# Kernel tuning notes

Hardware: AMD Instinct MI355X
Metric: run time of the kernel (lower is better)

## Reference

```python
import jax, jax.numpy as jnp
import numpy as np

N = 3072
F_IN = 512
H1 = 256
HFC = 64
OUT_DIM = 16
NUM_POOL = 3
P_CUT = 30.0  # ps[0]: percentile threshold on positive attention entries
CC_ITERS = 16  # min-label propagation w/ pointer jumping; reach >= 2^16 hops


def l2norm(x):
    # torch F.normalize(p=2, dim=1)
    return x / jnp.clip(jnp.linalg.norm(x, axis=1, keepdims=True), 1e-12, None)


def gcn(x, adj, W, b):
    # standard Kipf GraphConvolution: adj @ (x @ W) + b
    return adj @ (x @ W) + b


def normalize_adj(adj, k):
    n = adj.shape[0]
    A = adj + k * jnp.eye(n, dtype=adj.dtype)
    D = jnp.sqrt(A.sum(0))
    return A / (D[:, None] * D[None, :])


def edge_score(x, adj, a, W, b):
    h = x @ W + b                               # (n, HFC)
    s1 = h @ a[:HFC]                            # (n,)
    s2 = h @ a[HFC:]
    e = jax.nn.sigmoid(s1[:, None] + s2[None, :])
    att = jnp.where(adj > 0, e, jnp.zeros((), e.dtype))
    att = 0.5 * (att + att.T)
    i = jnp.arange(att.shape[0])
    return att.at[i, i].set(1.0)


def percentile_pos(att, p):
    # np.percentile(att[att>0], p) with linear interpolation, jit-safe
    pos = att > 0
    n_pos = pos.sum()
    s = jnp.sort(jnp.where(pos, att, jnp.inf).ravel())
    idx = (n_pos - 1).astype(att.dtype) * (p / 100.0)
    lo = jnp.floor(idx).astype(jnp.int32)
    hi = jnp.ceil(idx).astype(jnp.int32)
    frac = idx - lo.astype(att.dtype)
    return s[lo] * (1.0 - frac) + s[hi] * frac


def cc_labels(mask):
    # connected components via min-label propagation + pointer jumping.
    # diag of mask is always True (att diag = 1), so every node has a neighbor.
    n = mask.shape[0]
    def step(labels, _):
        neigh = jnp.min(jnp.where(mask, labels[None, :], n), axis=1)
        new = jnp.minimum(labels, neigh)
        new = new[new]  # pointer jumping doubles reach each iter
        return new, None
    labels, _ = jax.lax.scan(step, jnp.arange(n, dtype=jnp.int32), None, length=CC_ITERS)
    return labels


def pool(x, adj, att, p):
    cut = percentile_pos(att, p)
    att = att * (att >= cut).astype(att.dtype)
    labels = jax.lax.stop_gradient(cc_labels(att > 0))
    # fixed-shape membership: cluster id = representative (min) node index, padded to N
    C = jax.nn.one_hot(labels, att.shape[0], dtype=x.dtype).T  # (n_clusters=n, n)
    a2 = C @ adj @ C.T
    a2 = 0.5 * (a2 + a2.T)
    cnt = (att > 0).sum(1).astype(x.dtype)  # >=1 since diag survives the cut
    x2 = C @ ((att / cnt[:, None]) @ x)
    return x2, a2, C


def forward(x, adjC, adj, encW0, encb0, encW, encb, fcW, fcb, aW, decW, decb, decW_out, decb_out):
    adjs = [adj]
    adjCs = [adjC]
    xs, Cs, atts = [], [], []
    # ----- encode -----
    for k in range(NUM_POOL):
        x1 = x
        W, b = (encW0, encb0) if k == 0 else (encW[k - 1], encb[k - 1])
        h = jax.nn.relu(gcn(x, adjCs[-1], W, b))
        x = l2norm(h) if k == 0 else l2norm(h + x1)  # residual added for layer idx > 0
        xs.append(x)
        att = edge_score(x, adjs[-1], aW[k], fcW[k], fcb[k])
        x, adjk, C = pool(x, adjs[-1], att, P_CUT)
        adjCk = normalize_adj(adjk, 1.0)  # pool's adjC output is discarded in the original
        x = l2norm(x)
        adjs.append(adjk)
        adjCs.append(adjCk)
        atts.append(att)
        Cs.append(C)
    x = l2norm(jax.nn.elu(gcn(x, adjCs[-1], encW[NUM_POOL - 1], encb[NUM_POOL - 1])))
    xs.append(x)
    # ----- decode -----
    for k in range(NUM_POOL):
        lev = NUM_POOL - k - 1
        x = Cs[lev].T @ x                       # unpool; C is already binary
        x = jnp.concatenate([x, xs[lev]], axis=1)
        x = l2norm(jax.nn.elu(gcn(x, adjCs[lev], decW[k], decb[k])))
    x = gcn(x, adjCs[0], decW_out, decb_out)
    logp = jax.nn.log_softmax(x, axis=1)
    return logp, jnp.stack(Cs), jnp.stack(atts)


def setup_inputs() -> dict:
    key = jax.random.key(0)
    ks = jax.random.split(key, 12)
    x = jax.random.normal(ks[0], (N, F_IN), jnp.float32)
    u = jax.random.uniform(ks[1], (N, N))
    m = (u < 16.0 / N).astype(jnp.float32)  # avg degree ~16
    adj = jnp.maximum(m, m.T)
    i = jnp.arange(N)
    adj = adj.at[i, i].set(1.0)
    adjC = normalize_adj(adj, 1.0)

    def xav(k, shape):
        fan_in = shape[-2] if len(shape) > 1 else shape[-1]
        return jax.random.normal(k, shape, jnp.float32) * (1.0 / np.sqrt(fan_in))

    return {
        "x": x, "adjC": adjC, "adj": adj,
        "encW0": xav(ks[2], (F_IN, H1)), "encb0": jnp.zeros((H1,), jnp.float32),
        "encW": xav(ks[3], (NUM_POOL, H1, H1)), "encb": jnp.zeros((NUM_POOL, H1), jnp.float32),
        "fcW": xav(ks[4], (NUM_POOL, H1, HFC)), "fcb": jnp.zeros((NUM_POOL, HFC), jnp.float32),
        "aW": xav(ks[5], (NUM_POOL, 2 * HFC)),
        "decW": xav(ks[6], (NUM_POOL, 2 * H1, H1)), "decb": jnp.zeros((NUM_POOL, H1), jnp.float32),
        "decW_out": xav(ks[7], (H1, OUT_DIM)), "decb_out": jnp.zeros((OUT_DIM,), jnp.float32),
    }


def reference(x, adjC, adj, encW0, encb0, encW, encb, fcW, fcb, aW, decW, decb, decW_out, decb_out):
    return forward(x, adjC, adj, encW0, encb0, encW, encb, fcW, fcb, aW, decW, decb, decW_out, decb_out)
```

## Files before the change

kernel.cpp:

```cpp
#include <hip/hip_runtime.h>
#include <math.h>

#define NN 3072
#define FF 256
#define CAPE (1<<18)
#define MAXCH 3200

struct Scal {
  int nnzS, nnz2, nzero, mtot, ncht;
  int lo, hi, rank_rem, below_acc, c_le;
  unsigned prefix, vlo, minabove;
  float frac, cut;
};

__device__ __forceinline__ float sigm(float x){ return 1.0f/(1.0f+expf(-x)); }

__global__ __launch_bounds__(256) void k_count_dense(const float* __restrict__ A, int* __restrict__ rowcnt, float* __restrict__ Drow){
  int i=blockIdx.x, t=threadIdx.x;
  int c=0; float sm=0.f;
  for(int j=t;j<NN;j+=256){ float a=A[(size_t)i*NN+j]; if(a!=0.0f||j==i) c++; sm+=a; }
  __shared__ int s[256]; __shared__ float fs[256];
  s[t]=c; fs[t]=sm; __syncthreads();
  for(int o=128;o;o>>=1){ if(t<o){ s[t]+=s[t+o]; fs[t]+=fs[t+o]; } __syncthreads(); }
  if(t==0){ rowcnt[i]=s[0]; if(Drow) Drow[i]=sqrtf(fs[0]+1.0f); }
}

__global__ __launch_bounds__(1024) void k_scan(const int* __restrict__ cnt, int* __restrict__ rp, int* __restrict__ total){
  int t=threadIdx.x;
  int a0=cnt[t*3+0], a1=cnt[t*3+1], a2=cnt[t*3+2];
  int loc=a0+a1+a2;
  __shared__ int s[1024];
  s[t]=loc; __syncthreads();
  for(int o=1;o<1024;o<<=1){ int v=(t>=o)?s[t-o]:0; __syncthreads(); s[t]+=v; __syncthreads(); }
  int excl=s[t]-loc;
  rp[t*3+0]=excl; rp[t*3+1]=excl+a0; rp[t*3+2]=excl+a0+a1;
  if(t==1023){ rp[NN]=s[t]; *total=s[t]; }
}

__global__ __launch_bounds__(256) void k_fill_dense(const float* __restrict__ A, const float* __restrict__ ACd, const float* __restrict__ D,
    const int* __restrict__ rp, int* __restrict__ rows, int* __restrict__ cols, float* __restrict__ aval, float* __restrict__ acval){
  int i=blockIdx.x, t=threadIdx.x;
  const int CH=NN/256;
  int j0=t*CH; int c=0;
  for(int u=0;u<CH;u++){ int j=j0+u; float a=A[(size_t)i*NN+j]; if(a!=0.0f||j==i) c++; }
  __shared__ int s[256]; s[t]=c; __syncthreads();
  for(int o=1;o<256;o<<=1){ int v=(t>=o)?s[t-o]:0; __syncthreads(); s[t]+=v; __syncthreads(); }
  int pos=rp[i]+s[t]-c;
  float Di = D?D[i]:0.0f;
  for(int u=0;u<CH;u++){ int j=j0+u; float a=A[(size_t)i*NN+j];
    if(a!=0.0f||j==i){
      if(pos<CAPE){
        rows[pos]=i; cols[pos]=j; aval[pos]=a;
        acval[pos]= ACd? ACd[(size_t)i*NN+j] : (a+(j==i?1.0f:0.0f))/(Di*D[j]);
      }
      pos++;
    }
  }
}

__global__ __launch_bounds__(256) void k_gemm(const float* __restrict__ A, const float* __restrict__ B, float* __restrict__ C,
                                              int M, int K, int Nc){
  __shared__ float As[16][68];
  __shared__ float Bs[16][68];
  int tid=threadIdx.x;
  int tx=tid&15, ty=tid>>4;
  int bm=blockIdx.y*64, bn=blockIdx.x*64;
  int lm=tid>>2, lk=(tid&3)*4;
  int kr=tid>>4, nf=(tid&15)*4;
  float acc[4][4]={};
  for(int k0=0;k0<K;k0+=16){
    float4 a4=*(const float4*)(A+(size_t)(bm+lm)*K+k0+lk);
    As[lk+0][lm]=a4.x; As[lk+1][lm]=a4.y; As[lk+2][lm]=a4.z; As[lk+3][lm]=a4.w;
    float4 b4=*(const float4*)(B+(size_t)(k0+kr)*Nc+bn+nf);
    *(float4*)&Bs[kr][nf]=b4;
    __syncthreads();
#pragma unroll
    for(int kk=0;kk<16;kk++){
      float4 av=*(const float4*)&As[kk][ty*4];
      float4 bv=*(const float4*)&Bs[kk][tx*4];
      float am[4]={av.x,av.y,av.z,av.w};
      float bb[4]={bv.x,bv.y,bv.z,bv.w};
#pragma unroll
      for(int i2=0;i2<4;i2++)
#pragma unroll
        for(int j2=0;j2<4;j2++) acc[i2][j2]+=am[i2]*bb[j2];
    }
    __syncthreads();
  }
  for(int i2=0;i2<4;i2++){
    float4 o=make_float4(acc[i2][0],acc[i2][1],acc[i2][2],acc[i2][3]);
    *(float4*)(C+(size_t)(bm+ty*4+i2)*Nc+bn+tx*4)=o;
  }
}

__global__ __launch_bounds__(256) void k_gemm16(const float* __restrict__ X, const float* __restrict__ W, float* __restrict__ T){
  int idx=blockIdx.x*256+threadIdx.x;
  if(idx>=NN*16) return;
  int i=idx>>4, o=idx&15;
  float s=0.f;
  for(int kk=0;kk<FF;kk++) s+=X[(size_t)i*FF+kk]*W[kk*16+o];
  T[idx]=s;
}

__global__ __launch_bounds__(256) void k_spmm_gcn(const int* __restrict__ rp, const int* __restrict__ cols, const float* __restrict__ vals,
    const float* __restrict__ X, const float* __restrict__ bias, const float* __restrict__ resid, float* __restrict__ out, int act){
  int wid=blockIdx.x*4+(threadIdx.x>>6);
  int lane=threadIdx.x&63;
  if(wid>=NN) return;
  int e0=rp[wid], e1=rp[wid+1];
  float4 acc=make_float4(0,0,0,0);
  for(int e=e0;e<e1;e++){
    float v=vals[e]; int c=cols[e];
    float4 xv=*(const float4*)(X+(size_t)c*FF+lane*4);
    acc.x+=v*xv.x; acc.y+=v*xv.y; acc.z+=v*xv.z; acc.w+=v*xv.w;
  }
  float4 bv=*(const float4*)(bias+lane*4);
  acc.x+=bv.x; acc.y+=bv.y; acc.z+=bv.z; acc.w+=bv.w;
  if(act==0){
    acc.x=fmaxf(acc.x,0.f); acc.y=fmaxf(acc.y,0.f); acc.z=fmaxf(acc.z,0.f); acc.w=fmaxf(acc.w,0.f);
  } else {
    acc.x=acc.x>0.f?acc.x:expm1f(acc.x); acc.y=acc.y>0.f?acc.y:expm1f(acc.y);
    acc.z=acc.z>0.f?acc.z:expm1f(acc.z); acc.w=acc.w>0.f?acc.w:expm1f(acc.w);
  }
  if(resid){
    float4 r=*(const float4*)(resid+(size_t)wid*FF+lane*4);
    acc.x+=r.x; acc.y+=r.y; acc.z+=r.z; acc.w+=r.w;
  }
  float ss=acc.x*acc.x+acc.y*acc.y+acc.z*acc.z+acc.w*acc.w;
  for(int o=32;o;o>>=1) ss+=__shfl_xor(ss,o);
  float nrm=fmaxf(sqrtf(ss),1e-12f);
  float4 o4=make_float4(acc.x/nrm,acc.y/nrm,acc.z/nrm,acc.w/nrm);
  *(float4*)(out+(size_t)wid*FF+lane*4)=o4;
}

__global__ __launch_bounds__(256) void k_spmm_plain(const int* __restrict__ rp, const int* __restrict__ cols, const float* __restrict__ vals,
    const float* __restrict__ X, float* __restrict__ out){
  int wid=blockIdx.x*4+(threadIdx.x>>6);
  int lane=threadIdx.x&63;
  if(wid>=NN) return;
  int e0=rp[wid], e1=rp[wid+1];
  float4 acc=make_float4(0,0,0,0);
  for(int e=e0;e<e1;e++){
    if(e>=CAPE) break;
    float v=vals[e]; int c=cols[e];
    float4 xv=*(const float4*)(X+(size_t)c*FF+lane*4);
    acc.x+=v*xv.x; acc.y+=v*xv.y; acc.z+=v*xv.z; acc.w+=v*xv.w;
  }
  *(float4*)(out+(size_t)wid*FF+lane*4)=acc;
}

__global__ __launch_bounds__(64) void k_edge(const float* __restrict__ X, const float* __restrict__ fw, const float* __restrict__ fb,
    const float* __restrict__ av, float* __restrict__ s1, float* __restrict__ s2, Scal* sc){
  int i=blockIdx.x, l=threadIdx.x;
  if(i==0&&l==0) sc->nzero=0;
  __shared__ float xr[FF];
  *(float4*)&xr[l*4]=*(const float4*)(X+(size_t)i*FF+l*4);
  __syncthreads();
  float h=fb[l];
  for(int kk=0;kk<FF;kk++) h+=xr[kk]*fw[kk*64+l];
  float p1=h*av[l], p2=h*av[64+l];
  for(int o=32;o;o>>=1){ p1+=__shfl_xor(p1,o); p2+=__shfl_xor(p2,o); }
  if(l==0){ s1[i]=p1; s2[i]=p2; }
}

__global__ __launch_bounds__(256) void k_att_row(const int* __restrict__ rp, const int* __restrict__ cols,
    const float* __restrict__ s1, const float* __restrict__ s2, float* __restrict__ attD, float* __restrict__ cand, Scal* sc){
  __shared__ float row[NN];
  __shared__ int wred[4];
  int i=blockIdx.x, t=threadIdx.x;
  for(int j=t;j<NN;j+=256) row[j]=0.f;
  __syncthreads();
  int e0=rp[i], e1=rp[i+1];
  float s1i=s1[i], s2i=s2[i];
  int nz=0;
  for(int e=e0+t;e<e1;e+=256){
    int j=cols[e];
    float v=(j==i)?1.0f:0.5f*(sigm(s1i+s2[j])+sigm(s1[j]+s2i));
    row[j]=v;
    if(e<CAPE) cand[e]=v;
    if(!(v>0.f)) nz++;
  }
  for(int o=32;o;o>>=1) nz+=__shfl_xor(nz,o);
  if((t&63)==0) wred[t>>6]=nz;
  __syncthreads();
  if(t==0){ int s=wred[0]+wred[1]+wred[2]+wred[3]; if(s) atomicAdd(&sc->nzero,s); }
  float* orow=attD+(size_t)i*NN;
  for(int j=t*4;j<NN;j+=1024) *(float4*)(orow+j)=*(const float4*)&row[j];
}

__global__ void k_prep(Scal* sc){
  int np=sc->nnzS - sc->nzero;
  float idx=(float)(np-1)*(30.0f/100.0f);
  float fl=floorf(idx), ce=ceilf(idx);
  sc->lo=(int)fl; sc->hi=(int)ce; sc->frac=idx-fl;
  sc->rank_rem=sc->lo;
  sc->below_acc=0;
  sc->minabove=0xFFFFFFFFu;
}

template<int PHASE>
__global__ __launch_bounds__(256) void k_hist(const float* __restrict__ cand, const Scal* __restrict__ sc, unsigned* __restrict__ bins){
  const int NB = (PHASE==0)?16384:256;
  __shared__ unsigned h[NB];
  int t=threadIdx.x;
  for(int b=t;b<NB;b+=256) h[b]=0;
  __syncthreads();
  int n=sc->nnzS; if(n>CAPE) n=CAPE;
  unsigned pref=sc->prefix;
  int stride=gridDim.x*256;
  for(int e=blockIdx.x*256+t; e<n; e+=stride){
    float v=cand[e];
    if(!(v>0.f)) continue;
    unsigned bb=__float_as_uint(v);
    if(PHASE==0) atomicAdd(&h[bb>>16],1u);
    else if(PHASE==1){ if((bb>>16)==pref) atomicAdd(&h[(bb>>8)&0xFFu],1u); }
    else { if((bb>>8)==pref) atomicAdd(&h[bb&0xFFu],1u); }
  }
  __syncthreads();
  for(int b=t;b<NB;b+=256){ unsigned c=h[b]; if(c) atomicAdd(&bins[b],c); }
}

template<int PHASE>
__global__ __launch_bounds__(256) void k_pick(const unsigned* __restrict__ bins, Scal* sc){
  const int NB=(PHASE==0)?16384:256;
  const int PER=NB/256;
  __shared__ int part[256];
  __shared__ int selbin; __shared__ int below_sel;
  int t=threadIdx.x;
  int b0=t*PER;
  int sum=0;
  for(int u=0;u<PER;u++) sum+=(int)bins[b0+u];
  part[t]=sum; __syncthreads();
  for(int o=1;o<256;o<<=1){ int v=(t>=o)?part[t-o]:0; __syncthreads(); part[t]+=v; __syncthreads(); }
  int incl=part[t], excl=incl-sum;
  int r=sc->rank_rem;
  if(r>=excl && r<incl){
    int run=excl;
    for(int u=0;u<PER;u++){
      int c=(int)bins[b0+u];
      if(r<run+c){ selbin=b0+u; below_sel=run; break; }
      run+=c;
    }
  }
  __syncthreads();
  if(t==0){
    sc->rank_rem=r-below_sel;
    sc->below_acc+=below_sel;
    if(PHASE==0) sc->prefix=(unsigned)selbin;
    else if(PHASE==1) sc->prefix=(sc->prefix<<8)|(unsigned)selbin;
    else{
      sc->vlo=(sc->prefix<<8)|(unsigned)selbin;
      sc->c_le=sc->below_acc+(int)bins[selbin];
    }
  }
}

__global__ __launch_bounds__(256) void k_minabove(const float* __restrict__ cand, Scal* sc){
  int n=sc->nnzS; if(n>CAPE) n=CAPE;
  unsigned vlo=sc->vlo;
  int tid=threadIdx.x, lane=tid&63;
  int stride=gridDim.x*256;
  for(int base=blockIdx.x*256; base<n; base+=stride){
    int e=base+tid;
    unsigned b=0xFFFFFFFFu;
    if(e<n){ float v=cand[e]; if(v>0.f){ unsigned bb=__float_as_uint(v); if(bb>vlo) b=bb; } }
    for(int o=32;o;o>>=1){ unsigned ob=__shfl_xor(b,o); b=ob<b?ob:b; }
    if(lane==0&&b!=0xFFFFFFFFu) atomicMin(&sc->minabove,b);
  }
}

__global__ void k_cut(Scal* sc){
  float slo=__uint_as_float(sc->vlo);
  float shi;
  if(sc->hi==sc->lo) shi=slo;
  else if(sc->c_le>sc->hi) shi=slo;
  else shi=__uint_as_float(sc->minabove);
  sc->cut=slo*(1.0f-sc->frac)+shi*sc->frac;
}

__global__ __launch_bounds__(256) void k_pc_count(const int* __restrict__ rp, const float* __restrict__ cand, const Scal* __restrict__ sc,
    int* __restrict__ rowcnt, float* __restrict__ cntf){
  int wid=blockIdx.x*4+(threadIdx.x>>6);
  int lane=threadIdx.x&63;
  if(wid>=NN) return;
  int e0=rp[wid], e1=rp[wid+1];
  float cut=sc->cut;
  int c=0;
  for(int e=e0+lane;e<e1;e+=64){ if(e<CAPE && cand[e]>=cut) c++; }
  for(int o=32;o;o>>=1) c+=__shfl_xor(c,o);
  if(lane==0){ rowcnt[wid]=c; cntf[wid]=(float)c; }
}

__global__ __launch_bounds__(256) void k_pc_fill(const int* __restrict__ rp, const int* __restrict__ cols, const float* __restrict__ cand,
    const Scal* __restrict__ sc, const int* __restrict__ rp2, int* __restrict__ rows2, int* __restrict__ cols2, float* __restrict__ pval,
    const float* __restrict__ cntf){
  int wid=blockIdx.x*4+(threadIdx.x>>6);
  int lane=threadIdx.x&63;
  if(wid>=NN) return;
  int e0=rp[wid], e1=rp[wid+1];
  float cut=sc->cut, cf=cntf[wid];
  int base=rp2[wid];
  for(int eb=e0;eb<e1;eb+=64){
    int e=eb+lane;
    bool p=(e<e1)&&(e<CAPE)&&(cand[e]>=cut);
    unsigned long long m=__ballot(p);
    if(p){
      int pos=base+__popcll(m&((1ull<<lane)-1ull));
      if(pos<CAPE){ rows2[pos]=wid; cols2[pos]=cols[e]; pval[pos]=cand[e]/cf; }
    }
    base+=__popcll(m);
  }
}

__global__ __launch_bounds__(1024) void k_cc(const int* __restrict__ rows2, const int* __restrict__ cols2, Scal* sc,
    int* __restrict__ labk, int* __restrict__ moff_g, int* __restrict__ memb,
    int* __restrict__ choff_g, int* __restrict__ chm0_g, int* __restrict__ chm1_g){
  __shared__ int lab[NN];
  __shared__ int cnt[NN];
  __shared__ int mof[NN];
  __shared__ int s[1024];
  __shared__ int chg;
  int t=threadIdx.x;
  for(int i=t;i<NN;i+=1024){ lab[i]=i; cnt[i]=0; }
  int n2=sc->nnz2; if(n2>CAPE) n2=CAPE;
  __syncthreads();
  for(int it=0;it<16;it++){
    if(t==0) chg=0;
    __syncthreads();
    for(int e=t;e<n2;e+=1024){
      int i=rows2[e], j=cols2[e];
      if(i!=j){
        int li=lab[i], lj=lab[j];
        if(lj<li){ if(atomicMin(&lab[i],lj)>lj) chg=1; }
        else if(li<lj){ if(atomicMin(&lab[j],li)>li) chg=1; }
      }
    }
    __syncthreads();
    int l0=lab[t], l1=lab[t+1024], l2=lab[t+2048];
    int v0=lab[l0], v1=lab[l1], v2=lab[l2];
    __syncthreads();
    if(v0<l0){ lab[t]=v0; chg=1; }
    if(v1<l1){ lab[t+1024]=v1; chg=1; }
    if(v2<l2){ lab[t+2048]=v2; chg=1; }
    __syncthreads();
    if(!chg) break;
    __syncthreads();
  }
  for(int i=t;i<NN;i+=1024){ int l=lab[i]; labk[i]=l; atomicAdd(&cnt[l],1); }
  __syncthreads();
  int a0=cnt[t*3+0], a1=cnt[t*3+1], a2=cnt[t*3+2];
  int loc=a0+a1+a2;
  s[t]=loc; __syncthreads();
  for(int o=1;o<1024;o<<=1){ int v=(t>=o)?s[t-o]:0; __syncthreads(); s[t]+=v; __syncthreads(); }
  int excl=s[t]-loc;
  __syncthreads();
  mof[t*3+0]=excl; mof[t*3+1]=excl+a0; mof[t*3+2]=excl+a0+a1;
  cnt[t*3+0]=excl; cnt[t*3+1]=excl+a0; cnt[t*3+2]=excl+a0+a1;
  moff_g[t*3+0]=excl; moff_g[t*3+1]=excl+a0; moff_g[t*3+2]=excl+a0+a1;
  if(t==1023) moff_g[NN]=s[t];
  __syncthreads();
  int ch0=(a0+63)>>6, ch1=(a1+63)>>6, ch2=(a2+63)>>6;
  int locc=ch0+ch1+ch2;
  s[t]=locc; __syncthreads();
  for(int o=1;o<1024;o<<=1){ int v=(t>=o)?s[t-o]:0; __syncthreads(); s[t]+=v; __syncthreads(); }
  int cexcl=s[t]-locc;
  choff_g[t*3+0]=cexcl; choff_g[t*3+1]=cexcl+ch0; choff_g[t*3+2]=cexcl+ch0+ch1;
  if(t==1023){ choff_g[NN]=s[t]; sc->ncht=s[t]; }
  {
    int bases[3]={cexcl,cexcl+ch0,cexcl+ch0+ch1};
    int cnts[3]={a0,a1,a2};
    int nqs[3]={ch0,ch1,ch2};
    for(int u=0;u<3;u++){
      int m0=mof[t*3+u];
      int me=m0+cnts[u];
      for(int q=0;q<nqs[u];q++){
        int idx=bases[u]+q;
        if(idx<MAXCH){
          chm0_g[idx]=m0+q*64;
          int e2=m0+q*64+64; chm1_g[idx]=e2<me?e2:me;
        }
      }
    }
  }
  __syncthreads();
  int lane=t&63, wv=t>>6;
  for(int b=0;b<3;b++){
    int j=b*1024+t;
    int myl=lab[j];
    int rank_w=0,total=0;
#pragma unroll
    for(int l=0;l<64;l++){
      int lb=__shfl(myl,l);
      if(lb==myl){ total++; if(l<lane) rank_w++; }
    }
    for(int w=0;w<16;w++){
      if(wv==w){
        int base=cnt[myl];
        memb[base+rank_w]=j;
        if(rank_w==0) cnt[myl]=base+total;
      }
      __syncthreads();
    }
  }
}

__global__ __launch_bounds__(256) void k_a2e(const int* __restrict__ rowsA, const int* __restrict__ colsA_, const float* __restrict__ aval,
    const Scal* __restrict__ sc, const int* __restrict__ labk, float* __restrict__ dense){
  int e=blockIdx.x*256+threadIdx.x;
  int n=sc->nnzS; if(n>CAPE) n=CAPE;
  int lane=threadIdx.x&63;
  bool valid=(e<n);
  float a=valid?aval[e]:0.f;
  valid=valid&&(a!=0.f);
  int key=0;
  if(valid) key=labk[rowsA[e]]*NN+labk[colsA_[e]];
  unsigned long long act=__ballot(valid);
  while(act){
    int leader=__ffsll(act)-1;
    int lkey=__shfl(key,leader);
    bool same=valid&&(key==lkey);
    float contrib=same?a:0.f;
    for(int o=32;o;o>>=1) contrib+=__shfl_xor(contrib,o);
    if(lane==leader) atomicAdd(&dense[(size_t)lkey],contrib);
    act&=~__ballot(same);
  }
}

__global__ __launch_bounds__(256) void k_x2p(const float* __restrict__ y, const int* __restrict__ memb,
    const int* __restrict__ chm0, const int* __restrict__ chm1, const Scal* __restrict__ sc, float* __restrict__ partial){
  int b=blockIdx.x;
  if(b>=sc->ncht||b>=MAXCH) return;
  int t=threadIdx.x;
  int m0=chm0[b], m1=chm1[b];
  float acc=0.f;
#pragma unroll 4
  for(int m=m0;m<m1;m++) acc+=y[(size_t)memb[m]*FF+t];
  partial[(size_t)b*FF+t]=acc;
}
__global__ __launch_bounds__(256) void k_x2f(const int* __restrict__ choff, const float* __restrict__ partial, float* __restrict__ out){
  int c=blockIdx.x, t=threadIdx.x;
  int q0=choff[c], q1=choff[c+1];
  float acc=0.f;
  for(int q=q0;q<q1&&q<MAXCH;q++) acc+=partial[(size_t)q*FF+t];
  __shared__ float red[256];
  red[t]=acc*acc; __syncthreads();
  for(int o=128;o;o>>=1){ if(t<o) red[t]+=red[t+o]; __syncthreads(); }
  float nrm=fmaxf(sqrtf(red[0]),1e-12f);
  out[(size_t)c*FF+t]=(q1>q0)?acc/nrm:0.f;
}

__global__ __launch_bounds__(256) void k_gather(const float* __restrict__ X, const int* __restrict__ labs, const float* __restrict__ xsk,
    float* __restrict__ xcat){
  int idx=blockIdx.x*256+threadIdx.x;
  if(idx>=NN*128) return;
  int j=idx>>7, f4=idx&127;
  float4 v;
  if(f4<64) v=*(const float4*)(X+(size_t)labs[j]*FF+f4*4);
  else v=*(const float4*)(xsk+(size_t)j*FF+(size_t)(f4-64)*4);
  *(float4*)(xcat+(size_t)j*512+(size_t)f4*4)=v;
}

__global__ __launch_bounds__(256) void k_final(const int* __restrict__ rp, const int* __restrict__ cols, const float* __restrict__ vals,
    const float* __restrict__ T, const float* __restrict__ bias, float* __restrict__ logp){
  int i=blockIdx.x*256+threadIdx.x;
  if(i>=NN) return;
  float o[16];
#pragma unroll
  for(int f=0;f<16;f++) o[f]=bias[f];
  int e1=rp[i+1];
  for(int e=rp[i];e<e1;e++){
    float v=vals[e]; const float* tr=T+(size_t)cols[e]*16;
#pragma unroll
    for(int f=0;f<16;f++) o[f]+=v*tr[f];
  }
  float m=o[0];
#pragma unroll
  for(int f=1;f<16;f++) m=fmaxf(m,o[f]);
  float ssum=0.f;
#pragma unroll
  for(int f=0;f<16;f++) ssum+=expf(o[f]-m);
  float lse=logf(ssum);
#pragma unroll
  for(int f=0;f<16;f++) logp[(size_t)i*16+f]=o[f]-m-lse;
}

__global__ __launch_bounds__(256) void k_cfill(const int* __restrict__ labsv, float* __restrict__ CsB){
  int idx=blockIdx.x*256+threadIdx.x;
  if(idx>=3*NN) return;
  int l=idx/NN, j=idx-l*NN;
  int c=labsv[l*NN+j];
  CsB[(size_t)l*NN*NN+(size_t)c*NN+j]=1.0f;
}

extern "C" void kernel_launch(void* const* d_in, const int* in_sizes, int n_in,
                              void* d_out, int out_size, void* d_ws, size_t ws_size,
                              hipStream_t stream) {
  (void)in_sizes; (void)n_in; (void)out_size;
  const float* x_in =(const float*)d_in[0];
  const float* adjC =(const float*)d_in[1];
  const float* adj  =(const float*)d_in[2];
  const float* encW0=(const float*)d_in[3];
  const float* encb0=(const float*)d_in[4];
  const float* encW =(const float*)d_in[5];
  const float* encb =(const float*)d_in[6];
  const float* fcW  =(const float*)d_in[7];
  const float* fcb  =(const float*)d_in[8];
  const float* aW   =(const float*)d_in[9];
  const float* decW =(const float*)d_in[10];
  const float* decb =(const float*)d_in[11];
  const float* decWo=(const float*)d_in[12];
  const float* decbo=(const float*)d_in[13];
  float* out=(float*)d_out;

  float* logp=out;
  float* CsB = out + (size_t)NN*16;
  float* attB= CsB + 3ull*NN*NN;
  float* slot1 = CsB + (size_t)NN*NN;
  float* xs[4]; for(int i=0;i<4;i++) xs[i]=slot1+(size_t)i*NN*FF;
  float* xcur=slot1+(size_t)4*NN*FF;
  float* ybuf=slot1+(size_t)5*NN*FF;
  float* tbuf=slot1+(size_t)6*NN*FF;
  float* slot2 = CsB + 2ull*NN*NN;
  float* xcat=slot2;
  float* t16 = xcat + (size_t)NN*512;

  char* w=(char*)d_ws; size_t off=0;
  auto alc=[&](size_t b)->void*{ off=(off+255)&~(size_t)255; void* r=w+off; off+=b; return r; };
  Scal* sc=(Scal*)alc(sizeof(Scal));
  int* rowcnt=(int*)alc((size_t)NN*4);
  int* rp[4]; for(int i=0;i<4;i++) rp[i]=(int*)alc((size_t)(NN+1)*4);
  int* rp2=(int*)alc((size_t)(NN+1)*4);
  int* colsA[4]; float* acv[4];
  for(int i=0;i<4;i++){ colsA[i]=(int*)alc((size_t)CAPE*4); acv[i]=(float*)alc((size_t)CAPE*4); }
  float* avalS=(float*)alc((size_t)CAPE*4);
  int* rowsA=(int*)alc((size_t)CAPE*4);
  float* cand=(float*)alc((size_t)CAPE*4);
  int* rows2=(int*)alc((size_t)CAPE*4);
  int* cols2=(int*)alc((size_t)CAPE*4);
  float* pval=(float*)alc((size_t)CAPE*4);
  unsigned* bins=(unsigned*)alc((size_t)16384*4);
  int* labsv=(int*)alc((size_t)3*NN*4);
  int* moff=(int*)alc((size_t)(NN+1)*4);
  int* memb=(int*)alc((size_t)NN*4);
  int* choff=(int*)alc((size_t)(NN+1)*4);
  int* chm0=(int*)alc((size_t)MAXCH*4);
  int* chm1=(int*)alc((size_t)MAXCH*4);
  float* partial=(float*)alc((size_t)MAXCH*FF*4);
  float* cntf=(float*)alc((size_t)NN*4);
  float* s1=(float*)alc((size_t)NN*4);
  float* s2v=(float*)alc((size_t)NN*4);
  float* Dv=(float*)alc((size_t)NN*4);
  float* dense;
  size_t denseB=(size_t)NN*NN*4;
  if(ws_size>=off+denseB+4096) dense=(float*)alc(denseB);
  else dense=CsB;

  auto build_csr=[&](const float* Ad, const float* ACd, const float* Dp, int lvl){
    k_count_dense<<<NN,256,0,stream>>>(Ad,rowcnt,Dv);
    k_scan<<<1,1024,0,stream>>>(rowcnt,rp[lvl],&sc->nnzS);
    k_fill_dense<<<NN,256,0,stream>>>(Ad,ACd,Dp,rp[lvl],rowsA,colsA[lvl],avalS,acv[lvl]);
  };

  build_csr(adj,adjC,nullptr,0);

  for(int k=0;k<3;k++){
    const float* xin=(k==0)?x_in:xcur;
    const float* Wk=(k==0)?encW0:(encW+(size_t)(k-1)*FF*FF);
    const float* bk=(k==0)?encb0:(encb+(size_t)(k-1)*FF);
    int K=(k==0)?512:FF;
    k_gemm<<<dim3(FF/64,NN/64),256,0,stream>>>(xin,Wk,tbuf,NN,K,FF);
    k_spmm_gcn<<<NN/4,256,0,stream>>>(rp[k],colsA[k],acv[k],tbuf,bk,(k==0)?nullptr:xcur,xs[k],0);

    k_edge<<<NN,64,0,stream>>>(xs[k],fcW+(size_t)k*FF*64,fcb+(size_t)k*64,aW+(size_t)k*128,s1,s2v,sc);
    k_att_row<<<NN,256,0,stream>>>(rp[k],colsA[k],s1,s2v,attB+(size_t)k*NN*NN,cand,sc);

    k_prep<<<1,1,0,stream>>>(sc);
    hipMemsetAsync(bins,0,(size_t)16384*4,stream);
    k_hist<0><<<64,256,0,stream>>>(cand,sc,bins);
    k_pick<0><<<1,256,0,stream>>>(bins,sc);
    hipMemsetAsync(bins,0,(size_t)256*4,stream);
    k_hist<1><<<64,256,0,stream>>>(cand,sc,bins);
    k_pick<1><<<1,256,0,stream>>>(bins,sc);
    hipMemsetAsync(bins,0,(size_t)256*4,stream);
    k_hist<2><<<64,256,0,stream>>>(cand,sc,bins);
    k_pick<2><<<1,256,0,stream>>>(bins,sc);
    k_minabove<<<256,256,0,stream>>>(cand,sc);
    k_cut<<<1,1,0,stream>>>(sc);

    k_pc_count<<<NN/4,256,0,stream>>>(rp[k],cand,sc,rowcnt,cntf);
    k_scan<<<1,1024,0,stream>>>(rowcnt,rp2,&sc->nnz2);
    k_pc_fill<<<NN/4,256,0,stream>>>(rp[k],colsA[k],cand,sc,rp2,rows2,cols2,pval,cntf);

    k_cc<<<1,1024,0,stream>>>(rows2,cols2,sc,labsv+(size_t)k*NN,moff,memb,choff,chm0,chm1);

    hipMemsetAsync(dense,0,denseB,stream);
    k_a2e<<<CAPE/256,256,0,stream>>>(rowsA,colsA[k],avalS,sc,labsv+(size_t)k*NN,dense);

    k_spmm_plain<<<NN/4,256,0,stream>>>(rp2,cols2,pval,xs[k],ybuf);
    k_x2p<<<MAXCH,256,0,stream>>>(ybuf,memb,chm0,chm1,sc,partial);
    k_x2f<<<NN,256,0,stream>>>(choff,partial,xcur);

    build_csr(dense,nullptr,Dv,k+1);
  }

  k_gemm<<<dim3(FF/64,NN/64),256,0,stream>>>(xcur,encW+(size_t)2*FF*FF,tbuf,NN,FF,FF);
  k_spmm_gcn<<<NN/4,256,0,stream>>>(rp[3],colsA[3],acv[3],tbuf,encb+(size_t)2*FF,nullptr,xs[3],1);

  float* xd=xs[3];
  float* outsb[3]={xcur,ybuf,xcur};
  for(int k=0;k<3;k++){
    int lev=2-k;
    k_gather<<<(NN*128)/256,256,0,stream>>>(xd,labsv+(size_t)lev*NN,xs[lev],xcat);
    k_gemm<<<dim3(FF/64,NN/64),256,0,stream>>>(xcat,decW+(size_t)k*512*FF,tbuf,NN,512,FF);
    k_spmm_gcn<<<NN/4,256,0,stream>>>(rp[lev],colsA[lev],acv[lev],tbuf,decb+(size_t)k*FF,nullptr,outsb[k],1);
    xd=outsb[k];
  }

  k_gemm16<<<(NN*16)/256,256,0,stream>>>(xd,decWo,t16);
  k_final<<<(NN+255)/256,256,0,stream>>>(rp[0],colsA[0],acv[0],t16,decbo,logp);

  hipMemsetAsync(CsB,0,3ull*NN*NN*4,stream);
  k_cfill<<<(3*NN+255)/256,256,0,stream>>>(labsv,CsB);
}
```

Measured before the change: 915.7 us.

## Split-K GEMM with atomics, fold percentile prep into pick, hash-aggregate edge coarsening

The dense GEMM is now split along K into two halves over a z-grid and accumulates into a zeroed output with float atomics, which doubles block count on a small grid. The percentile setup kernel and two bin memsets are folded into the pick kernels. Edge-to-cluster aggregation now uses a per-block shared-memory hash table with integer counts before flushing to global memory, replacing the wave-level ballot loop. Risks: nondeterministic summation order, an extra memset per GEMM, and the hash path truncates edge values to unsigned integers, which only holds if adjacency weights are integral.

```diff
diff --git a/kernel.cpp b/kernel.cpp
--- a/kernel.cpp
+++ b/kernel.cpp
@@ -5,6 +5,7 @@
 #define FF 256
 #define CAPE (1<<18)
 #define MAXCH 3200
+#define HSZ 2048
 
 struct Scal {
   int nnzS, nnz2, nzero, mtot, ncht;
@@ -65,10 +66,12 @@
   int tid=threadIdx.x;
   int tx=tid&15, ty=tid>>4;
   int bm=blockIdx.y*64, bn=blockIdx.x*64;
+  int kh=K>>1;
+  int kbeg=blockIdx.z*kh, kend=kbeg+kh;
   int lm=tid>>2, lk=(tid&3)*4;
   int kr=tid>>4, nf=(tid&15)*4;
   float acc[4][4]={};
-  for(int k0=0;k0<K;k0+=16){
+  for(int k0=kbeg;k0<kend;k0+=16){
     float4 a4=*(const float4*)(A+(size_t)(bm+lm)*K+k0+lk);
     As[lk+0][lm]=a4.x; As[lk+1][lm]=a4.y; As[lk+2][lm]=a4.z; As[lk+3][lm]=a4.w;
     float4 b4=*(const float4*)(B+(size_t)(k0+kr)*Nc+bn+nf);
@@ -87,10 +90,11 @@
     }
     __syncthreads();
   }
-  for(int i2=0;i2<4;i2++){
-    float4 o=make_float4(acc[i2][0],acc[i2][1],acc[i2][2],acc[i2][3]);
-    *(float4*)(C+(size_t)(bm+ty*4+i2)*Nc+bn+tx*4)=o;
-  }
+#pragma unroll
+  for(int i2=0;i2<4;i2++)
+#pragma unroll
+    for(int j2=0;j2<4;j2++)
+      atomicAdd(C+(size_t)(bm+ty*4+i2)*Nc+bn+tx*4+j2, acc[i2][j2]);
 }
 
 __global__ __launch_bounds__(256) void k_gemm16(const float* __restrict__ X, const float* __restrict__ W, float* __restrict__ T){
@@ -188,16 +192,6 @@
   for(int j=t*4;j<NN;j+=1024) *(float4*)(orow+j)=*(const float4*)&row[j];
 }
 
-__global__ void k_prep(Scal* sc){
-  int np=sc->nnzS - sc->nzero;
-  float idx=(float)(np-1)*(30.0f/100.0f);
-  float fl=floorf(idx), ce=ceilf(idx);
-  sc->lo=(int)fl; sc->hi=(int)ce; sc->frac=idx-fl;
-  sc->rank_rem=sc->lo;
-  sc->below_acc=0;
-  sc->minabove=0xFFFFFFFFu;
-}
-
 template<int PHASE>
 __global__ __launch_bounds__(256) void k_hist(const float* __restrict__ cand, const Scal* __restrict__ sc, unsigned* __restrict__ bins){
   const int NB = (PHASE==0)?16384:256;
@@ -221,19 +215,32 @@
 }
 
 template<int PHASE>
-__global__ __launch_bounds__(256) void k_pick(const unsigned* __restrict__ bins, Scal* sc){
+__global__ __launch_bounds__(256) void k_pick(unsigned* __restrict__ bins, Scal* sc){
   const int NB=(PHASE==0)?16384:256;
   const int PER=NB/256;
   __shared__ int part[256];
-  __shared__ int selbin; __shared__ int below_sel;
+  __shared__ int selbin; __shared__ int below_sel; __shared__ int sh_r;
   int t=threadIdx.x;
+  if(t==0){
+    int r;
+    if(PHASE==0){
+      int np=sc->nnzS - sc->nzero;
+      float idx=(float)(np-1)*(30.0f/100.0f);
+      float fl=floorf(idx), ce=ceilf(idx);
+      sc->lo=(int)fl; sc->hi=(int)ce; sc->frac=idx-fl;
+      sc->below_acc=0; sc->minabove=0xFFFFFFFFu;
+      r=(int)fl;
+    } else r=sc->rank_rem;
+    sh_r=r;
+  }
+  __syncthreads();
+  int r=sh_r;
   int b0=t*PER;
   int sum=0;
   for(int u=0;u<PER;u++) sum+=(int)bins[b0+u];
   part[t]=sum; __syncthreads();
   for(int o=1;o<256;o<<=1){ int v=(t>=o)?part[t-o]:0; __syncthreads(); part[t]+=v; __syncthreads(); }
   int incl=part[t], excl=incl-sum;
-  int r=sc->rank_rem;
   if(r>=excl && r<incl){
     int run=excl;
     for(int u=0;u<PER;u++){
@@ -252,6 +259,10 @@
       sc->vlo=(sc->prefix<<8)|(unsigned)selbin;
       sc->c_le=sc->below_acc+(int)bins[selbin];
     }
+  }
+  if(PHASE<2){
+    __syncthreads();
+    if(t<256) bins[t]=0;
   }
 }
 
@@ -406,23 +417,30 @@
 
 __global__ __launch_bounds__(256) void k_a2e(const int* __restrict__ rowsA, const int* __restrict__ colsA_, const float* __restrict__ aval,
     const Scal* __restrict__ sc, const int* __restrict__ labk, float* __restrict__ dense){
-  int e=blockIdx.x*256+threadIdx.x;
+  __shared__ int hkey[HSZ];
+  __shared__ unsigned hv[HSZ];
+  int t=threadIdx.x;
+  for(int i=t;i<HSZ;i+=256){ hkey[i]=-1; hv[i]=0; }
+  __syncthreads();
   int n=sc->nnzS; if(n>CAPE) n=CAPE;
-  int lane=threadIdx.x&63;
-  bool valid=(e<n);
-  float a=valid?aval[e]:0.f;
-  valid=valid&&(a!=0.f);
-  int key=0;
-  if(valid) key=labk[rowsA[e]]*NN+labk[colsA_[e]];
-  unsigned long long act=__ballot(valid);
-  while(act){
-    int leader=__ffsll(act)-1;
-    int lkey=__shfl(key,leader);
-    bool same=valid&&(key==lkey);
-    float contrib=same?a:0.f;
-    for(int o=32;o;o>>=1) contrib+=__shfl_xor(contrib,o);
-    if(lane==leader) atomicAdd(&dense[(size_t)lkey],contrib);
-    act&=~__ballot(same);
+  int e=blockIdx.x*256+t;
+  if(e<n){
+    float a=aval[e];
+    if(a!=0.f){
+      int key=labk[rowsA[e]]*NN+labk[colsA_[e]];
+      unsigned val=(unsigned)a;
+      unsigned hsh=((unsigned)key*2654435761u)&(HSZ-1);
+      for(;;){
+        int k0=atomicCAS(&hkey[hsh],-1,key);
+        if(k0==-1||k0==key){ atomicAdd(&hv[hsh],val); break; }
+        hsh=(hsh+1)&(HSZ-1);
+      }
+    }
+  }
+  __syncthreads();
+  for(int i=t;i<HSZ;i+=256){
+    int k0=hkey[i];
+    if(k0>=0) atomicAdd(&dense[(size_t)k0],(float)hv[i]);
   }
 }
 
@@ -561,6 +579,11 @@
     k_fill_dense<<<NN,256,0,stream>>>(Ad,ACd,Dp,rp[lvl],rowsA,colsA[lvl],avalS,acv[lvl]);
   };
 
+  auto gemm=[&](const float* A,const float* B,float* C,int K){
+    hipMemsetAsync(C,0,(size_t)NN*FF*4,stream);
+    k_gemm<<<dim3(FF/64,NN/64,2),256,0,stream>>>(A,B,C,NN,K,FF);
+  };
+
   build_csr(adj,adjC,nullptr,0);
 
   for(int k=0;k<3;k++){
@@ -568,20 +591,17 @@
     const float* Wk=(k==0)?encW0:(encW+(size_t)(k-1)*FF*FF);
     const float* bk=(k==0)?encb0:(encb+(size_t)(k-1)*FF);
     int K=(k==0)?512:FF;
-    k_gemm<<<dim3(FF/64,NN/64),256,0,stream>>>(xin,Wk,tbuf,NN,K,FF);
+    gemm(xin,Wk,tbuf,K);
     k_spmm_gcn<<<NN/4,256,0,stream>>>(rp[k],colsA[k],acv[k],tbuf,bk,(k==0)?nullptr:xcur,xs[k],0);
 
     k_edge<<<NN,64,0,stream>>>(xs[k],fcW+(size_t)k*FF*64,fcb+(size_t)k*64,aW+(size_t)k*128,s1,s2v,sc);
     k_att_row<<<NN,256,0,stream>>>(rp[k],colsA[k],s1,s2v,attB+(size_t)k*NN*NN,cand,sc);
 
-    k_prep<<<1,1,0,stream>>>(sc);
     hipMemsetAsync(bins,0,(size_t)16384*4,stream);
     k_hist<0><<<64,256,0,stream>>>(cand,sc,bins);
     k_pick<0><<<1,256,0,stream>>>(bins,sc);
-    hipMemsetAsync(bins,0,(size_t)256*4,stream);
     k_hist<1><<<64,256,0,stream>>>(cand,sc,bins);
     k_pick<1><<<1,256,0,stream>>>(bins,sc);
-    hipMemsetAsync(bins,0,(size_t)256*4,stream);
     k_hist<2><<<64,256,0,stream>>>(cand,sc,bins);
     k_pick<2><<<1,256,0,stream>>>(bins,sc);
     k_minabove<<<256,256,0,stream>>>(cand,sc);
@@ -603,7 +623,7 @@
     build_csr(dense,nullptr,Dv,k+1);
   }
 
-  k_gemm<<<dim3(FF/64,NN/64),256,0,stream>>>(xcur,encW+(size_t)2*FF*FF,tbuf,NN,FF,FF);
+  gemm(xcur,encW+(size_t)2*FF*FF,tbuf,FF);
   k_spmm_gcn<<<NN/4,256,0,stream>>>(rp[3],colsA[3],acv[3],tbuf,encb+(size_t)2*FF,nullptr,xs[3],1);
 
   float* xd=xs[3];
@@ -611,7 +631,7 @@
   for(int k=0;k<3;k++){
     int lev=2-k;
     k_gather<<<(NN*128)/256,256,0,stream>>>(xd,labsv+(size_t)lev*NN,xs[lev],xcat);
-    k_gemm<<<dim3(FF/64,NN/64),256,0,stream>>>(xcat,decW+(size_t)k*512*FF,tbuf,NN,512,FF);
+    gemm(xcat,decW+(size_t)k*512*FF,tbuf,512);
     k_spmm_gcn<<<NN/4,256,0,stream>>>(rp[lev],colsA[lev],acv[lev],tbuf,decb+(size_t)k*FF,nullptr,outsb[k],1);
     xd=outsb[k];
   }
```

Result: no change. 932.7 us (+1.9%).
